# Kernel tuning notes

Hardware: AMD Instinct MI355X
Metric: run time of the kernel (lower is better)

The kernel has to match this reference:

```python
import jax, jax.numpy as jnp
import numpy as np

N_NODES = 50000
N_EDGES = 600000
D_IN = 128
D_HID = D_IN // 2  # 64
OUT_CLASSES = 2


def setup_inputs() -> dict:
    key = jax.random.key(0)
    k_h, k_src, k_dst, k_w1, k_b1, k_w2, k_b2 = jax.random.split(key, 7)
    h = jax.random.normal(k_h, (N_NODES, D_IN), dtype=jnp.float32)
    src = jax.random.randint(k_src, (N_EDGES,), 0, N_NODES, dtype=jnp.int64)
    dst = jax.random.randint(k_dst, (N_EDGES,), 0, N_NODES, dtype=jnp.int64)
    # nn.Linear default init: U(-1/sqrt(fan_in), 1/sqrt(fan_in))
    lim1 = 1.0 / np.sqrt(D_IN)
    W1 = jax.random.uniform(k_w1, (D_IN, D_HID), minval=-lim1, maxval=lim1, dtype=jnp.float32)
    b1 = jax.random.uniform(k_b1, (D_HID,), minval=-lim1, maxval=lim1, dtype=jnp.float32)
    lim2 = 1.0 / np.sqrt(D_HID)
    W2 = jax.random.uniform(k_w2, (D_HID, OUT_CLASSES), minval=-lim2, maxval=lim2, dtype=jnp.float32)
    b2 = jax.random.uniform(k_b2, (OUT_CLASSES,), minval=-lim2, maxval=lim2, dtype=jnp.float32)
    return {"h": h, "W1": W1, "b1": b1, "W2": W2, "b2": b2, "src": src, "dst": dst}


def reference(h, W1, b1, W2, b2, src, dst):
    # Gather node features to edges, elementwise multiply, 2-layer MLP.
    e = h[src] * h[dst]                       # [E, D_IN]
    hid = jax.nn.relu(e @ W1 + b1)            # [E, D_HID]
    score = hid @ W2 + b2                     # [E, OUT_CLASSES]
    return score
```

## Files before the change

kernel.cpp:

```cpp
#include <hip/hip_runtime.h>
#include <hip/hip_bf16.h>


#define NEDGE 600000
#define NNODES 50000
#define DIN 128
#define DH 64
#define STRK 136
#define HCVT 6250
#define WCVT 8
#define MAINB 4688

typedef __attribute__((ext_vector_type(8))) short bf16x8;
typedef __attribute__((ext_vector_type(4))) float f32x4;
typedef __attribute__((ext_vector_type(4))) unsigned int u32x4;

static __device__ __forceinline__ short f2bf(float f) {
    __hip_bfloat16 hb = __float2bfloat16(f);
    return *reinterpret_cast<short*>(&hb);
}
static __device__ __forceinline__ float bflo(unsigned int w) {
    return __builtin_bit_cast(float, w << 16);
}
static __device__ __forceinline__ float bfhi(unsigned int w) {
    return __builtin_bit_cast(float, w & 0xffff0000u);
}

__global__ __launch_bounds__(256) void prep_kernel(
    const float* __restrict__ h, const float* __restrict__ W1,
    unsigned short* __restrict__ hbf, unsigned short* __restrict__ w1t, int wofs)
{
    const int b = blockIdx.x;
    if (b < wofs) {
        int i = (b * 256 + threadIdx.x) * 4;
        f32x4 v = *reinterpret_cast<const f32x4*>(h + i);
        ushort4 o;
        o.x = (unsigned short)f2bf(v[0]);
        o.y = (unsigned short)f2bf(v[1]);
        o.z = (unsigned short)f2bf(v[2]);
        o.w = (unsigned short)f2bf(v[3]);
        *reinterpret_cast<ushort4*>(hbf + i) = o;
    } else {
        int j = ((b - wofs) * 256 + threadIdx.x) * 4;
        f32x4 w = *reinterpret_cast<const f32x4*>(W1 + j);
        int k = j >> 6, c = j & 63;
#pragma unroll
        for (int q = 0; q < 4; ++q)
            w1t[(c + q) * DIN + k] = (unsigned short)f2bf(w[q]);
    }
}

__global__ __launch_bounds__(256, 4) void mlp_main(
    const unsigned short* __restrict__ hbf,
    const unsigned short* __restrict__ w1t,
    const int* __restrict__ src, const int* __restrict__ dst,
    const float* __restrict__ b1, const float* __restrict__ W2,
    const float* __restrict__ b2, float* __restrict__ out)
{
    __shared__ unsigned short Blds[DH * STRK];

    const int tid = threadIdx.x;
    const int l = tid & 63;
    const int lr = l & 15;
    const int g = l >> 4;
    const unsigned kg = (unsigned)(g * 8);
    const int bpos = blockIdx.x * 128 + (tid >> 6) * 32;

    int p0 = bpos + lr;      if (p0 >= NEDGE) p0 = NEDGE - 1;
    int p1 = bpos + 16 + lr; if (p1 >= NEDGE) p1 = NEDGE - 1;
    const unsigned sa0 = (unsigned)src[p0] * (unsigned)DIN;
    const unsigned da0 = (unsigned)dst[p0] * (unsigned)DIN;
    const unsigned sa1 = (unsigned)src[p1] * (unsigned)DIN;
    const unsigned da1 = (unsigned)dst[p1] * (unsigned)DIN;

    u32x4 S0[4], D0[4], S1[4], D1[4];
#pragma unroll
    for (int ks = 0; ks < 4; ++ks) {
        S0[ks] = *reinterpret_cast<const u32x4*>(hbf + sa0 + ks * 32 + kg);
        D0[ks] = *reinterpret_cast<const u32x4*>(hbf + da0 + ks * 32 + kg);
        S1[ks] = *reinterpret_cast<const u32x4*>(hbf + sa1 + ks * 32 + kg);
        D1[ks] = *reinterpret_cast<const u32x4*>(hbf + da1 + ks * 32 + kg);
    }
    __builtin_amdgcn_sched_barrier(0);

#pragma unroll
    for (int j = 0; j < 4; ++j) {
        int i = (tid + j * 256) * 8;
        int r = i >> 7, c = i & 127;
        const ushort4* ps = reinterpret_cast<const ushort4*>(w1t + i);
        ushort4 v0 = ps[0], v1 = ps[1];
        *reinterpret_cast<ushort4*>(&Blds[r * STRK + c]) = v0;
        *reinterpret_cast<ushort4*>(&Blds[r * STRK + c + 4]) = v1;
    }
    __syncthreads();

    float bv[4]; float2 w2v[4];
#pragma unroll
    for (int n = 0; n < 4; ++n) {
        bv[n] = b1[n * 16 + lr];
        w2v[n] = *reinterpret_cast<const float2*>(W2 + (n * 16 + lr) * 2);
    }
    const float bb0 = b2[0], bb1 = b2[1];

    f32x4 acc[4];

#pragma unroll
    for (int n = 0; n < 4; ++n) acc[n] = (f32x4){bv[n], bv[n], bv[n], bv[n]};
#pragma unroll
    for (int ks = 0; ks < 4; ++ks) {
        bf16x8 A;
#pragma unroll
        for (int w = 0; w < 4; ++w) {
            A[2 * w]     = f2bf(bflo(S0[ks][w]) * bflo(D0[ks][w]));
            A[2 * w + 1] = f2bf(bfhi(S0[ks][w]) * bfhi(D0[ks][w]));
        }
#pragma unroll
        for (int n = 0; n < 4; ++n) {
            bf16x8 Bf = *reinterpret_cast<const bf16x8*>(
                &Blds[(n * 16 + lr) * STRK + ks * 32 + kg]);
            acc[n] = __builtin_amdgcn_mfma_f32_16x16x32_bf16(A, Bf, acc[n], 0, 0, 0);
        }
    }
    {
        float o0 = 0.f, o1 = 0.f;
#pragma unroll
        for (int r = 0; r < 4; ++r) {
            float q0 = 0.f, q1 = 0.f;
#pragma unroll
            for (int n = 0; n < 4; ++n) {
                float v = fmaxf(acc[n][r], 0.f);
                q0 = fmaf(v, w2v[n].x, q0);
                q1 = fmaf(v, w2v[n].y, q1);
            }
#pragma unroll
            for (int sh = 1; sh < 16; sh <<= 1) {
                q0 += __shfl_xor(q0, sh, 64);
                q1 += __shfl_xor(q1, sh, 64);
            }
            if (lr == r) { o0 = q0; o1 = q1; }
        }
        int epos = bpos + g * 4 + lr;
        if (lr < 4 && epos < NEDGE) {
            float2 ov = make_float2(o0 + bb0, o1 + bb1);
            *reinterpret_cast<float2*>(out + (size_t)epos * 2) = ov;
        }
    }

#pragma unroll
    for (int n = 0; n < 4; ++n) acc[n] = (f32x4){bv[n], bv[n], bv[n], bv[n]};
#pragma unroll
    for (int ks = 0; ks < 4; ++ks) {
        bf16x8 A;
#pragma unroll
        for (int w = 0; w < 4; ++w) {
            A[2 * w]     = f2bf(bflo(S1[ks][w]) * bflo(D1[ks][w]));
            A[2 * w + 1] = f2bf(bfhi(S1[ks][w]) * bfhi(D1[ks][w]));
        }
#pragma unroll
        for (int n = 0; n < 4; ++n) {
            bf16x8 Bf = *reinterpret_cast<const bf16x8*>(
                &Blds[(n * 16 + lr) * STRK + ks * 32 + kg]);
            acc[n] = __builtin_amdgcn_mfma_f32_16x16x32_bf16(A, Bf, acc[n], 0, 0, 0);
        }
    }
    {
        float o0 = 0.f, o1 = 0.f;
#pragma unroll
        for (int r = 0; r < 4; ++r) {
            float q0 = 0.f, q1 = 0.f;
#pragma unroll
            for (int n = 0; n < 4; ++n) {
                float v = fmaxf(acc[n][r], 0.f);
                q0 = fmaf(v, w2v[n].x, q0);
                q1 = fmaf(v, w2v[n].y, q1);
            }
#pragma unroll
            for (int sh = 1; sh < 16; sh <<= 1) {
                q0 += __shfl_xor(q0, sh, 64);
                q1 += __shfl_xor(q1, sh, 64);
            }
            if (lr == r) { o0 = q0; o1 = q1; }
        }
        int epos = bpos + 16 + g * 4 + lr;
        if (lr < 4 && epos < NEDGE) {
            float2 ov = make_float2(o0 + bb0, o1 + bb1);
            *reinterpret_cast<float2*>(out + (size_t)epos * 2) = ov;
        }
    }
}

__global__ __launch_bounds__(256) void mlp_f32_fallback(
    const float* __restrict__ hf, const unsigned short* __restrict__ w1t,
    const float* __restrict__ b1, const float* __restrict__ W2,
    const float* __restrict__ b2, const int* __restrict__ src,
    const int* __restrict__ dst, float* __restrict__ out)
{
    const int tid = threadIdx.x;
    const int l = tid & 63, lr = l & 15, g = l >> 4;
    const unsigned kg = (unsigned)(g * 8);
    const int wbase = blockIdx.x * 64 + (tid >> 6) * 16;
    const unsigned e = (unsigned)(wbase + lr);
    const unsigned sa = (unsigned)src[e] * (unsigned)DIN;
    const unsigned da = (unsigned)dst[e] * (unsigned)DIN;
    f32x4 acc[4];
#pragma unroll
    for (int n = 0; n < 4; ++n) {
        float bvv = b1[n * 16 + lr];
        acc[n] = (f32x4){bvv, bvv, bvv, bvv};
    }
#pragma unroll
    for (int ks = 0; ks < 4; ++ks) {
        const float* ps = hf + sa + ks * 128 + g * 32;
        const float* pd = hf + da + ks * 128 + g * 32;
        f32x4 s0 = *reinterpret_cast<const f32x4*>(ps);
        f32x4 s1 = *reinterpret_cast<const f32x4*>(ps + 4);
        f32x4 d0 = *reinterpret_cast<const f32x4*>(pd);
        f32x4 d1 = *reinterpret_cast<const f32x4*>(pd + 4);
        bf16x8 A, B[4];
#pragma unroll
        for (int n = 0; n < 4; ++n)
            B[n] = *reinterpret_cast<const bf16x8*>(w1t + (n * 16 + lr) * DIN + ks * 32 + kg);
#pragma unroll
        for (int q = 0; q < 4; ++q) {
            A[q]     = f2bf(s0[q] * d0[q]);
            A[q + 4] = f2bf(s1[q] * d1[q]);
        }
#pragma unroll
        for (int n = 0; n < 4; ++n)
            acc[n] = __builtin_amdgcn_mfma_f32_16x16x32_bf16(A, B[n], acc[n], 0, 0, 0);
    }
    float2 w2v[4];
#pragma unroll
    for (int n = 0; n < 4; ++n)
        w2v[n] = *reinterpret_cast<const float2*>(W2 + (n * 16 + lr) * 2);
    const float bb0 = b2[0], bb1 = b2[1];
    float o0 = 0.f, o1 = 0.f;
#pragma unroll
    for (int r = 0; r < 4; ++r) {
        float q0 = 0.f, q1 = 0.f;
#pragma unroll
        for (int n = 0; n < 4; ++n) {
            float v = fmaxf(acc[n][r], 0.f);
            q0 = fmaf(v, w2v[n].x, q0);
            q1 = fmaf(v, w2v[n].y, q1);
        }
#pragma unroll
        for (int sh = 1; sh < 16; sh <<= 1) {
            q0 += __shfl_xor(q0, sh, 64);
            q1 += __shfl_xor(q1, sh, 64);
        }
        if (lr == r) { o0 = q0; o1 = q1; }
    }
    if (lr < 4) {
        int edge = wbase + g * 4 + lr;
        float2 ov = make_float2(o0 + bb0, o1 + bb1);
        *reinterpret_cast<float2*>(out + (size_t)edge * 2) = ov;
    }
}

extern "C" void kernel_launch(void* const* d_in, const int* in_sizes, int n_in,
                              void* d_out, int out_size, void* d_ws, size_t ws_size,
                              hipStream_t stream) {
    const float* h  = (const float*)d_in[0];
    const float* W1 = (const float*)d_in[1];
    const float* b1 = (const float*)d_in[2];
    const float* W2 = (const float*)d_in[3];
    const float* b2 = (const float*)d_in[4];
    const int* src  = (const int*)d_in[5];
    const int* dst  = (const int*)d_in[6];
    float* out = (float*)d_out;

    const size_t OFF_W1T = (size_t)NNODES * DIN * 2;
    const size_t NEED_BF = OFF_W1T + (size_t)DH * DIN * 2;
    const size_t NEED_MIN = (size_t)DH * DIN * 2;

    char* ws = (char*)d_ws;

    if (ws_size >= NEED_BF) {
        unsigned short* hbf = (unsigned short*)ws;
        unsigned short* w1t = (unsigned short*)(ws + OFF_W1T);
        prep_kernel<<<HCVT + WCVT, 256, 0, stream>>>(h, W1, hbf, w1t, HCVT);
        mlp_main<<<MAINB, 256, 0, stream>>>(hbf, w1t, src, dst, b1, W2, b2, out);
    } else if (ws_size >= NEED_MIN) {
        unsigned short* w1t = (unsigned short*)ws;
        prep_kernel<<<WCVT, 256, 0, stream>>>(h, W1, nullptr, w1t, 0);
        mlp_f32_fallback<<<NEDGE / 64, 256, 0, stream>>>(h, w1t, b1, W2, b2, src, dst, out);
    }
}
```

Measured before the change: 61.36 us.

## Issue gathers via inline asm with partial waitcnt and transpose MFMA epilogue

Replaces compiler-scheduled gather loads with inline-asm global_load_dwordx4 using immediate offsets, moves them after the LDS weight staging, and waits with vmcnt(8) so the first edge group's MFMA and epilogue overlap the second group's loads. Swaps the MFMA operand order so each lane holds outputs for one edge, which cuts the epilogue shuffle reduction from a 16-lane butterfly to two xor shuffles. Bias and W2 are packed into shared memory as float4s. The inline asm relies on a hand-counted vmcnt, which is fragile if the compiler emits other vector memory ops in between.

```diff
diff --git a/kernel.cpp b/kernel.cpp
--- a/kernel.cpp
+++ b/kernel.cpp
@@ -50,6 +50,10 @@
     }
 }
 
+#define GLOAD(dst, voff, imm) \
+    asm volatile("global_load_dwordx4 %0, %1, %2 offset:" imm \
+                 : "=&v"(dst) : "v"(voff), "s"(hbf))
+
 __global__ __launch_bounds__(256, 4) void mlp_main(
     const unsigned short* __restrict__ hbf,
     const unsigned short* __restrict__ w1t,
@@ -58,6 +62,7 @@
     const float* __restrict__ b2, float* __restrict__ out)
 {
     __shared__ unsigned short Blds[DH * STRK];
+    __shared__ float4 Pack[DH];
 
     const int tid = threadIdx.x;
     const int l = tid & 63;
@@ -68,20 +73,10 @@
 
     int p0 = bpos + lr;      if (p0 >= NEDGE) p0 = NEDGE - 1;
     int p1 = bpos + 16 + lr; if (p1 >= NEDGE) p1 = NEDGE - 1;
-    const unsigned sa0 = (unsigned)src[p0] * (unsigned)DIN;
-    const unsigned da0 = (unsigned)dst[p0] * (unsigned)DIN;
-    const unsigned sa1 = (unsigned)src[p1] * (unsigned)DIN;
-    const unsigned da1 = (unsigned)dst[p1] * (unsigned)DIN;
-
-    u32x4 S0[4], D0[4], S1[4], D1[4];
-#pragma unroll
-    for (int ks = 0; ks < 4; ++ks) {
-        S0[ks] = *reinterpret_cast<const u32x4*>(hbf + sa0 + ks * 32 + kg);
-        D0[ks] = *reinterpret_cast<const u32x4*>(hbf + da0 + ks * 32 + kg);
-        S1[ks] = *reinterpret_cast<const u32x4*>(hbf + sa1 + ks * 32 + kg);
-        D1[ks] = *reinterpret_cast<const u32x4*>(hbf + da1 + ks * 32 + kg);
-    }
-    __builtin_amdgcn_sched_barrier(0);
+    const unsigned sb0 = ((unsigned)src[p0] * (unsigned)DIN + kg) * 2u;
+    const unsigned db0 = ((unsigned)dst[p0] * (unsigned)DIN + kg) * 2u;
+    const unsigned sb1 = ((unsigned)src[p1] * (unsigned)DIN + kg) * 2u;
+    const unsigned db1 = ((unsigned)dst[p1] * (unsigned)DIN + kg) * 2u;
 
 #pragma unroll
     for (int j = 0; j < 4; ++j) {
@@ -92,20 +87,30 @@
         *reinterpret_cast<ushort4*>(&Blds[r * STRK + c]) = v0;
         *reinterpret_cast<ushort4*>(&Blds[r * STRK + c + 4]) = v1;
     }
+    if (tid < DH) {
+        float2 w2 = *reinterpret_cast<const float2*>(W2 + tid * 2);
+        Pack[tid] = make_float4(b1[tid], w2.x, w2.y, 0.f);
+    }
+    const float bb0 = b2[0], bb1 = b2[1];
     __syncthreads();
 
-    float bv[4]; float2 w2v[4];
-#pragma unroll
-    for (int n = 0; n < 4; ++n) {
-        bv[n] = b1[n * 16 + lr];
-        w2v[n] = *reinterpret_cast<const float2*>(W2 + (n * 16 + lr) * 2);
-    }
-    const float bb0 = b2[0], bb1 = b2[1];
+    u32x4 S0[4], D0[4], S1[4], D1[4];
+    GLOAD(S0[0], sb0, "0");   GLOAD(S0[1], sb0, "64");
+    GLOAD(S0[2], sb0, "128"); GLOAD(S0[3], sb0, "192");
+    GLOAD(D0[0], db0, "0");   GLOAD(D0[1], db0, "64");
+    GLOAD(D0[2], db0, "128"); GLOAD(D0[3], db0, "192");
+    GLOAD(S1[0], sb1, "0");   GLOAD(S1[1], sb1, "64");
+    GLOAD(S1[2], sb1, "128"); GLOAD(S1[3], sb1, "192");
+    GLOAD(D1[0], db1, "0");   GLOAD(D1[1], db1, "64");
+    GLOAD(D1[2], db1, "128"); GLOAD(D1[3], db1, "192");
 
     f32x4 acc[4];
-
-#pragma unroll
-    for (int n = 0; n < 4; ++n) acc[n] = (f32x4){bv[n], bv[n], bv[n], bv[n]};
+    float o00, o01, o10, o11;
+
+    asm volatile("s_waitcnt vmcnt(8)" ::: "memory");
+    __builtin_amdgcn_sched_barrier(0);
+#pragma unroll
+    for (int n = 0; n < 4; ++n) acc[n] = (f32x4){0.f, 0.f, 0.f, 0.f};
 #pragma unroll
     for (int ks = 0; ks < 4; ++ks) {
         bf16x8 A;
@@ -116,38 +121,31 @@
         }
 #pragma unroll
         for (int n = 0; n < 4; ++n) {
-            bf16x8 Bf = *reinterpret_cast<const bf16x8*>(
+            bf16x8 Wf = *reinterpret_cast<const bf16x8*>(
                 &Blds[(n * 16 + lr) * STRK + ks * 32 + kg]);
-            acc[n] = __builtin_amdgcn_mfma_f32_16x16x32_bf16(A, Bf, acc[n], 0, 0, 0);
+            acc[n] = __builtin_amdgcn_mfma_f32_16x16x32_bf16(Wf, A, acc[n], 0, 0, 0);
         }
     }
     {
-        float o0 = 0.f, o1 = 0.f;
-#pragma unroll
-        for (int r = 0; r < 4; ++r) {
-            float q0 = 0.f, q1 = 0.f;
-#pragma unroll
-            for (int n = 0; n < 4; ++n) {
-                float v = fmaxf(acc[n][r], 0.f);
-                q0 = fmaf(v, w2v[n].x, q0);
-                q1 = fmaf(v, w2v[n].y, q1);
+        float q0 = 0.f, q1 = 0.f;
+#pragma unroll
+        for (int n = 0; n < 4; ++n)
+#pragma unroll
+            for (int r = 0; r < 4; ++r) {
+                float4 pw = Pack[n * 16 + g * 4 + r];
+                float v = fmaxf(acc[n][r] + pw.x, 0.f);
+                q0 = fmaf(v, pw.y, q0);
+                q1 = fmaf(v, pw.z, q1);
             }
-#pragma unroll
-            for (int sh = 1; sh < 16; sh <<= 1) {
-                q0 += __shfl_xor(q0, sh, 64);
-                q1 += __shfl_xor(q1, sh, 64);
-            }
-            if (lr == r) { o0 = q0; o1 = q1; }
-        }
-        int epos = bpos + g * 4 + lr;
-        if (lr < 4 && epos < NEDGE) {
-            float2 ov = make_float2(o0 + bb0, o1 + bb1);
-            *reinterpret_cast<float2*>(out + (size_t)epos * 2) = ov;
-        }
-    }
-
-#pragma unroll
-    for (int n = 0; n < 4; ++n) acc[n] = (f32x4){bv[n], bv[n], bv[n], bv[n]};
+        q0 += __shfl_xor(q0, 16, 64); q0 += __shfl_xor(q0, 32, 64);
+        q1 += __shfl_xor(q1, 16, 64); q1 += __shfl_xor(q1, 32, 64);
+        o00 = q0 + bb0; o01 = q1 + bb1;
+    }
+
+    asm volatile("s_waitcnt vmcnt(0)" ::: "memory");
+    __builtin_amdgcn_sched_barrier(0);
+#pragma unroll
+    for (int n = 0; n < 4; ++n) acc[n] = (f32x4){0.f, 0.f, 0.f, 0.f};
 #pragma unroll
     for (int ks = 0; ks < 4; ++ks) {
         bf16x8 A;
@@ -158,34 +156,34 @@
         }
 #pragma unroll
         for (int n = 0; n < 4; ++n) {
-            bf16x8 Bf = *reinterpret_cast<const bf16x8*>(
+            bf16x8 Wf = *reinterpret_cast<const bf16x8*>(
                 &Blds[(n * 16 + lr) * STRK + ks * 32 + kg]);
-            acc[n] = __builtin_amdgcn_mfma_f32_16x16x32_bf16(A, Bf, acc[n], 0, 0, 0);
+            acc[n] = __builtin_amdgcn_mfma_f32_16x16x32_bf16(Wf, A, acc[n], 0, 0, 0);
         }
     }
     {
-        float o0 = 0.f, o1 = 0.f;
-#pragma unroll
-        for (int r = 0; r < 4; ++r) {
-            float q0 = 0.f, q1 = 0.f;
-#pragma unroll
-            for (int n = 0; n < 4; ++n) {
-                float v = fmaxf(acc[n][r], 0.f);
-                q0 = fmaf(v, w2v[n].x, q0);
-                q1 = fmaf(v, w2v[n].y, q1);
+        float q0 = 0.f, q1 = 0.f;
+#pragma unroll
+        for (int n = 0; n < 4; ++n)
+#pragma unroll
+            for (int r = 0; r < 4; ++r) {
+                float4 pw = Pack[n * 16 + g * 4 + r];
+                float v = fmaxf(acc[n][r] + pw.x, 0.f);
+                q0 = fmaf(v, pw.y, q0);
+                q1 = fmaf(v, pw.z, q1);
             }
-#pragma unroll
-            for (int sh = 1; sh < 16; sh <<= 1) {
-                q0 += __shfl_xor(q0, sh, 64);
-                q1 += __shfl_xor(q1, sh, 64);
-            }
-            if (lr == r) { o0 = q0; o1 = q1; }
-        }
-        int epos = bpos + 16 + g * 4 + lr;
-        if (lr < 4 && epos < NEDGE) {
-            float2 ov = make_float2(o0 + bb0, o1 + bb1);
-            *reinterpret_cast<float2*>(out + (size_t)epos * 2) = ov;
-        }
+        q0 += __shfl_xor(q0, 16, 64); q0 += __shfl_xor(q0, 32, 64);
+        q1 += __shfl_xor(q1, 16, 64); q1 += __shfl_xor(q1, 32, 64);
+        o10 = q0 + bb0; o11 = q1 + bb1;
+    }
+
+    if (l < 16) {
+        int e0 = bpos + l;
+        if (e0 < NEDGE)
+            *reinterpret_cast<float2*>(out + (size_t)e0 * 2) = make_float2(o00, o01);
+        int e1 = bpos + 16 + l;
+        if (e1 < NEDGE)
+            *reinterpret_cast<float2*>(out + (size_t)e1 * 2) = make_float2(o10, o11);
     }
 }
 
```

Result: faster. 56.22 us (-8.4%).
